# Kernel tuning notes

Measured on AMD Instinct MI355X. Metric: run time of the kernel, lower is better.

The kernel has to match this reference:

```python
import jax, jax.numpy as jnp
import numpy as np

B, SEQ, C, H = 4, 1024, 256, 4
Dk = C // H                                  # 64
L = 4 * SEQ                                  # 4096 attention length
FACTOR = 4
N_TOP = FACTOR * int(np.ceil(np.log(L)))     # U = 36 dominant queries
SAMPLE_K = FACTOR * int(np.ceil(np.log(L)))  # u = 36 sampled keys per query


def _forward(et, mp, co, vol, Wq, bq, Wk, bk, Wv, bv, Wo, bo, index_sample):
    sz = et.shape[0]
    # student_graph input shuffle (faithful to the torch .view calls)
    x = jnp.concatenate([et.reshape(SEQ, -1), co.reshape(SEQ, -1),
                         mp.reshape(SEQ, -1), vol.reshape(SEQ, -1)], axis=-1)
    x = x.reshape(sz, L, C)  # [B, 4*seq_len, d_model]
    # projections; ProbAttention uses view(B,H,L,-1) which is a raw reshape
    # (NOT a transpose) of the [B,L,H,Dk] tensor -> fuse into one reshape
    q = (x @ Wq + bq).reshape(sz, H, L, Dk)
    k = (x @ Wk + bk).reshape(sz, H, L, Dk)
    v = (x @ Wv + bv).reshape(sz, H, L, Dk)
    # _prob_QK: random key sampling + sparsity measure + top-k query select
    K_sample = k[:, :, index_sample, :]                        # [B,H,L,u,Dk]
    QKs = jnp.einsum('bhse,bhske->bhsk', q, K_sample)          # [B,H,L,u]
    M = QKs.max(axis=-1) - QKs.sum(axis=-1) / L                # [B,H,L]
    _, m_top = jax.lax.top_k(M, N_TOP)                         # [B,H,U]
    q_red = jnp.take_along_axis(q, m_top[..., None], axis=2)   # [B,H,U,Dk]
    scores = jnp.einsum('bhue,bhle->bhul', q_red, k) * (1.0 / float(np.sqrt(Dk)))
    attn = jax.nn.softmax(scores, axis=-1)                     # [B,H,U,L]
    upd = jnp.einsum('bhul,bhld->bhud', attn, v)               # [B,H,U,Dk]
    # initial context = V-sum broadcast; scatter dense update at top queries
    ctx = jnp.broadcast_to(v.sum(axis=2, keepdims=True), (sz, H, L, Dk))
    bi = jnp.arange(sz)[:, None, None]
    hi = jnp.arange(H)[None, :, None]
    ctx = ctx.at[bi, hi, m_top, :].set(upd)                    # [B,H,L,Dk]
    # AttentionLayer output: .view(B, L, -1) on contiguous [B,H,L,Dk] is again
    # a raw reshape (faithful), then out projection
    out = ctx.reshape(sz, L, H * Dk) @ Wo + bo                 # [B,L,C]
    return out.reshape(SEQ, -1)


def setup_inputs():
    key = jax.random.key(0)
    ks = jax.random.split(key, 13)
    f = lambda i, shp: jax.random.normal(ks[i], shp, jnp.float32)
    ws = 1.0 / float(np.sqrt(C))  # keep logits in a sane range
    return {
        'et': f(0, (B, SEQ, C)), 'mp': f(1, (B, SEQ, C)),
        'co': f(2, (B, SEQ, C)), 'vol': f(3, (B, SEQ, C)),
        'Wq': f(4, (C, C)) * ws, 'bq': f(5, (C,)) * 0.01,
        'Wk': f(6, (C, C)) * ws, 'bk': f(7, (C,)) * 0.01,
        'Wv': f(8, (C, C)) * ws, 'bv': f(9, (C,)) * 0.01,
        'Wo': f(10, (C, C)) * ws, 'bo': f(11, (C,)) * 0.01,
        'index_sample': jax.random.randint(ks[12], (L, SAMPLE_K), 0, L, dtype=jnp.int32),
        'comp_idx': 0,
    }


def reference(et, mp, co, vol, Wq, bq, Wk, bk, Wv, bv, Wo, bo, index_sample, comp_idx):
    return _forward(et, mp, co, vol, Wq, bq, Wk, bk, Wv, bv, Wo, bo, index_sample)
```

## Files before the change

kernel.cpp:

```cpp
#include <hip/hip_runtime.h>
#include <hip/hip_bf16.h>

#define BHn 16
#define Ln 4096
#define NTOP 36
#define SKn 36
#define NCHUNK 64

using s16x8 = __attribute__((ext_vector_type(8))) short;
using u16x8 = __attribute__((ext_vector_type(8))) unsigned short;
using f32x4 = __attribute__((ext_vector_type(4))) float;

__device__ __forceinline__ unsigned short bf_hi(float f) {
  unsigned u = __float_as_uint(f);
  return (unsigned short)((u + 0x7fffu + ((u >> 16) & 1u)) >> 16);
}

__global__ __launch_bounds__(256) void wconv(
    const float* __restrict__ W0, const float* __restrict__ W1, const float* __restrict__ W2,
    unsigned short* __restrict__ th0, unsigned short* __restrict__ tl0,
    unsigned short* __restrict__ th1, unsigned short* __restrict__ tl1,
    unsigned short* __restrict__ th2, unsigned short* __restrict__ tl2) {
  int wsel = blockIdx.y;
  const float* W = (wsel == 0) ? W0 : (wsel == 1) ? W1 : W2;
  unsigned short* TH = (wsel == 0) ? th0 : (wsel == 1) ? th1 : th2;
  unsigned short* TL = (wsel == 0) ? tl0 : (wsel == 1) ? tl1 : tl2;
  int kr = blockIdx.x * 16;
  int n = threadIdx.x;
  u16x8 hv[2], lv[2];
#pragma unroll
  for (int j = 0; j < 16; ++j) {
    float f = W[(size_t)(kr + j) * 256 + n];
    unsigned short h = bf_hi(f);
    float lof = f - __uint_as_float(((unsigned)h) << 16);
    hv[j >> 3][j & 7] = h;
    lv[j >> 3][j & 7] = bf_hi(lof);
  }
  *(u16x8*)&TH[(size_t)n * 256 + kr] = hv[0];
  *(u16x8*)&TH[(size_t)n * 256 + kr + 8] = hv[1];
  *(u16x8*)&TL[(size_t)n * 256 + kr] = lv[0];
  *(u16x8*)&TL[(size_t)n * 256 + kr + 8] = lv[1];
}

__global__ __launch_bounds__(256) void xconv(
    const float* __restrict__ s0, const float* __restrict__ s1,
    const float* __restrict__ s2, const float* __restrict__ s3,
    unsigned short* __restrict__ Axh, unsigned short* __restrict__ Axl) {
  int t = threadIdx.x;
  int row = blockIdx.x * 4 + (t >> 6);
  int c = t & 63;
  int l = row & 4095, b = row >> 12;
  int part = (l >> 2) & 3;
  int seq = ((l >> 4) << 2) | (l & 3);
  const float* sp = (part == 0) ? s0 : (part == 1) ? s1 : (part == 2) ? s2 : s3;
  float4 f = ((const float4*)(sp + (size_t)((b << 10) + seq) * 256))[c];
  float fv[4] = {f.x, f.y, f.z, f.w};
  ushort4 hv, lv;
  unsigned short* hp = (unsigned short*)&hv;
  unsigned short* lp = (unsigned short*)&lv;
#pragma unroll
  for (int j = 0; j < 4; ++j) {
    unsigned short h = bf_hi(fv[j]);
    float lof = fv[j] - __uint_as_float(((unsigned)h) << 16);
    hp[j] = h;
    lp[j] = bf_hi(lof);
  }
  *(ushort4*)&Axh[(size_t)row * 256 + c * 4] = hv;
  *(ushort4*)&Axl[(size_t)row * 256 + c * 4] = lv;
}

#define LDW 40
__global__ __launch_bounds__(256, 3) void qkv_mfma(
    const unsigned short* __restrict__ Axh, const unsigned short* __restrict__ Axl,
    const unsigned short* __restrict__ th0, const unsigned short* __restrict__ tl0,
    const unsigned short* __restrict__ th1, const unsigned short* __restrict__ tl1,
    const unsigned short* __restrict__ th2, const unsigned short* __restrict__ tl2,
    const float* __restrict__ b0, const float* __restrict__ b1, const float* __restrict__ b2,
    float* __restrict__ o0, float* __restrict__ o1, float* __restrict__ o2) {
  __shared__ __align__(16) unsigned short Ah[128 * LDW];
  __shared__ __align__(16) unsigned short Al[128 * LDW];
  __shared__ __align__(16) unsigned short Bh[128 * LDW];
  __shared__ __align__(16) unsigned short Bl[128 * LDW];
  int t = threadIdx.x;
  int wsel = blockIdx.x >> 1;
  int col0 = (blockIdx.x & 1) * 128;
  int row0 = blockIdx.y * 128;
  const unsigned short* TH = (wsel == 0) ? th0 : (wsel == 1) ? th1 : th2;
  const unsigned short* TL = (wsel == 0) ? tl0 : (wsel == 1) ? tl1 : tl2;
  const float* bias = (wsel == 0) ? b0 : (wsel == 1) ? b1 : b2;
  float* O = (wsel == 0) ? o0 : (wsel == 1) ? o1 : o2;

  int srow = t >> 1, half = t & 1;
  const unsigned short* ah_g = Axh + (size_t)(row0 + srow) * 256 + half * 16;
  const unsigned short* al_g = Axl + (size_t)(row0 + srow) * 256 + half * 16;
  const unsigned short* bh_g = TH + (size_t)(col0 + srow) * 256 + half * 16;
  const unsigned short* bl_g = TL + (size_t)(col0 + srow) * 256 + half * 16;

  int lane = t & 63;
  int wv = t >> 6;
  int wr = wv >> 1, wc = wv & 1;
  int fr = lane & 15, fk = lane >> 4;
  int aoff = (wr * 64 + fr) * LDW + fk * 8;
  int boff = (wc * 64 + fr) * LDW + fk * 8;

  f32x4 acc[4][4] = {};

  for (int k0 = 0; k0 < 256; k0 += 32) {
    int wa = srow * LDW + half * 16;
    u16x8 va0 = *(const u16x8*)(ah_g + k0);
    u16x8 va1 = *(const u16x8*)(ah_g + k0 + 8);
    u16x8 vl0 = *(const u16x8*)(al_g + k0);
    u16x8 vl1 = *(const u16x8*)(al_g + k0 + 8);
    u16x8 vb0 = *(const u16x8*)(bh_g + k0);
    u16x8 vb1 = *(const u16x8*)(bh_g + k0 + 8);
    u16x8 vc0 = *(const u16x8*)(bl_g + k0);
    u16x8 vc1 = *(const u16x8*)(bl_g + k0 + 8);
    *(u16x8*)&Ah[wa] = va0; *(u16x8*)&Ah[wa + 8] = va1;
    *(u16x8*)&Al[wa] = vl0; *(u16x8*)&Al[wa + 8] = vl1;
    *(u16x8*)&Bh[wa] = vb0; *(u16x8*)&Bh[wa + 8] = vb1;
    *(u16x8*)&Bl[wa] = vc0; *(u16x8*)&Bl[wa + 8] = vc1;
    __syncthreads();

    s16x8 fah[4], fal[4];
#pragma unroll
    for (int mi = 0; mi < 4; ++mi) {
      fah[mi] = *(const s16x8*)&Ah[aoff + mi * 16 * LDW];
      fal[mi] = *(const s16x8*)&Al[aoff + mi * 16 * LDW];
    }
#pragma unroll
    for (int ni = 0; ni < 4; ++ni) {
      s16x8 fbh = *(const s16x8*)&Bh[boff + ni * 16 * LDW];
      s16x8 fbl = *(const s16x8*)&Bl[boff + ni * 16 * LDW];
#pragma unroll
      for (int mi = 0; mi < 4; ++mi) {
        acc[mi][ni] = __builtin_amdgcn_mfma_f32_16x16x32_bf16(fah[mi], fbh, acc[mi][ni], 0, 0, 0);
        acc[mi][ni] = __builtin_amdgcn_mfma_f32_16x16x32_bf16(fal[mi], fbh, acc[mi][ni], 0, 0, 0);
        acc[mi][ni] = __builtin_amdgcn_mfma_f32_16x16x32_bf16(fah[mi], fbl, acc[mi][ni], 0, 0, 0);
      }
    }
    __syncthreads();
  }

#pragma unroll
  for (int ni = 0; ni < 4; ++ni) {
    int n = col0 + wc * 64 + ni * 16 + fr;
    float bv = bias[n];
#pragma unroll
    for (int mi = 0; mi < 4; ++mi) {
      int mb = row0 + wr * 64 + mi * 16 + fk * 4;
#pragma unroll
      for (int r = 0; r < 4; ++r)
        O[(size_t)(mb + r) * 256 + n] = acc[mi][ni][r] + bv;
    }
  }
}

__global__ __launch_bounds__(256) void qks_m3(
    const float* __restrict__ q, const float* __restrict__ k,
    const int* __restrict__ idxs, float* __restrict__ Mout) {
  __shared__ float qs[64][68];
  __shared__ int il[64 * SKn];
  int g = blockIdx.x;
  int x = g & 7;
  int i = g >> 3;
  int bh = (x << 1) | (i >> 6);
  int s0 = (i & 63) * 64;
  int t = threadIdx.x;
  size_t base = (size_t)bh << 12;
  for (int i2 = t; i2 < 1024; i2 += 256) {
    int row = i2 >> 4, d4 = i2 & 15;
    *(float4*)&qs[row][d4 * 4] = ((const float4*)(q + (base + s0 + row) * 64))[d4];
  }
  for (int i2 = t; i2 < 64 * SKn; i2 += 256) il[i2] = idxs[s0 * SKn + i2];
  __syncthreads();
  int sl = t >> 2;
  int dq = t & 3;
  float qr[16];
#pragma unroll
  for (int i2 = 0; i2 < 4; ++i2)
    *(float4*)&qr[i2 * 4] = *(const float4*)&qs[sl][i2 * 16 + dq * 4];
  float mx = -INFINITY, sm = 0.f;
  const float4* kb4 = (const float4*)(k + base * 64);
#pragma unroll 4
  for (int j = 0; j < SKn; ++j) {
    int l = il[sl * SKn + j];
    const float4* kr = kb4 + (size_t)l * 16;
    float acc = 0.f;
#pragma unroll
    for (int i2 = 0; i2 < 4; ++i2) {
      float4 kv = kr[i2 * 4 + dq];
      acc += kv.x * qr[i2 * 4] + kv.y * qr[i2 * 4 + 1] + kv.z * qr[i2 * 4 + 2] + kv.w * qr[i2 * 4 + 3];
    }
    acc += __shfl_xor(acc, 1, 64);
    acc += __shfl_xor(acc, 2, 64);
    mx = fmaxf(mx, acc);
    sm += acc;
  }
  if (dq == 0) Mout[base + s0 + sl] = mx - sm * (1.0f / 4096.0f);
}

__global__ __launch_bounds__(256) void topk_radix(
    const float* __restrict__ M, int* __restrict__ topidx) {
  __shared__ unsigned hist[4096];
  __shared__ unsigned sup[256];
  __shared__ unsigned cand_u[256];
  __shared__ int cand_i[256];
  __shared__ int s_bin1, s_bin2, s_above, s_ocnt, s_ccnt;
  int bh = blockIdx.x;
  int t = threadIdx.x;
  int mbase = bh * 4096;
  unsigned uv[16];
  for (int i = t; i < 4096; i += 256) hist[i] = 0;
  __syncthreads();
#pragma unroll
  for (int r = 0; r < 16; ++r) {
    unsigned b = __float_as_uint(M[mbase + t + 256 * r]);
    unsigned u = b ^ ((unsigned)((int)b >> 31) | 0x80000000u);
    uv[r] = u;
    atomicAdd(&hist[u >> 20], 1u);
  }
  __syncthreads();
  {
    unsigned ssum = 0;
    for (int i = 0; i < 16; ++i) ssum += hist[t * 16 + i];
    sup[t] = ssum;
  }
  __syncthreads();
  if (t == 0) {
    unsigned cum = 0; int sb = 255;
    for (; sb > 0; --sb) { if (cum + sup[sb] >= NTOP) break; cum += sup[sb]; }
    int b = sb * 16 + 15;
    for (; b > sb * 16; --b) { if (cum + hist[b] >= NTOP) break; cum += hist[b]; }
    s_bin1 = b; s_above = (int)cum;
  }
  __syncthreads();
  int bin1 = s_bin1;
  int need1 = NTOP - s_above;
  __syncthreads();
  for (int i = t; i < 4096; i += 256) hist[i] = 0;
  __syncthreads();
#pragma unroll
  for (int r = 0; r < 16; ++r)
    if ((int)(uv[r] >> 20) == bin1) atomicAdd(&hist[(uv[r] >> 8) & 0xFFF], 1u);
  __syncthreads();
  {
    unsigned ssum = 0;
    for (int i = 0; i < 16; ++i) ssum += hist[t * 16 + i];
    sup[t] = ssum;
  }
  __syncthreads();
  if (t == 0) {
    unsigned cum = 0; int sb = 255;
    for (; sb > 0; --sb) { if (cum + sup[sb] >= (unsigned)need1) break; cum += sup[sb]; }
    int b = sb * 16 + 15;
    for (; b > sb * 16; --b) { if (cum + hist[b] >= (unsigned)need1) break; cum += hist[b]; }
    s_bin2 = b; s_above += (int)cum;
    s_ocnt = 0; s_ccnt = 0;
  }
  __syncthreads();
  int bin2 = s_bin2;
  int need = NTOP - s_above;
  int* outp = topidx + bh * NTOP;
#pragma unroll
  for (int r = 0; r < 16; ++r) {
    unsigned u = uv[r];
    int b1 = u >> 20, b2 = (u >> 8) & 0xFFF;
    if (b1 > bin1 || (b1 == bin1 && b2 > bin2)) {
      int p = atomicAdd(&s_ocnt, 1);
      outp[p] = t + 256 * r;
    } else if (b1 == bin1 && b2 == bin2) {
      int p = atomicAdd(&s_ccnt, 1);
      if (p < 256) { cand_u[p] = u; cand_i[p] = t + 256 * r; }
    }
  }
  __syncthreads();
  if (t == 0) {
    int cc = s_ccnt < 256 ? s_ccnt : 256;
    int slot = s_ocnt;
    for (int n = 0; n < need; ++n) {
      unsigned bu = 0; int bi = 0x7fffffff, bp = -1;
      for (int c = 0; c < cc; ++c) {
        if (cand_i[c] < 0) continue;
        if (cand_u[c] > bu || (cand_u[c] == bu && cand_i[c] < bi)) {
          bu = cand_u[c]; bi = cand_i[c]; bp = c;
        }
      }
      outp[slot++] = bi;
      cand_i[bp] = -1;
    }
  }
}

__global__ __launch_bounds__(256) void vsum_partial(
    const float* __restrict__ v, float* __restrict__ part) {
  __shared__ float4 red[256];
  int bh = blockIdx.x, ch = blockIdx.y;
  int t = threadIdx.x;
  int rg = t >> 4, d4 = t & 15;
  const float4* v4 = (const float4*)(v + ((size_t)bh * 4096 + ch * 256) * 64);
  float4 acc = {0.f, 0.f, 0.f, 0.f};
  for (int r = rg; r < 256; r += 16) {
    float4 x = v4[r * 16 + d4];
    acc.x += x.x; acc.y += x.y; acc.z += x.z; acc.w += x.w;
  }
  red[t] = acc;
  __syncthreads();
  for (int s2 = 8; s2 > 0; s2 >>= 1) {
    if (rg < s2) {
      float4 o = red[(rg + s2) * 16 + d4];
      red[t].x += o.x; red[t].y += o.y; red[t].z += o.z; red[t].w += o.w;
    }
    __syncthreads();
  }
  if (rg == 0) ((float4*)part)[((size_t)bh * 16 + ch) * 16 + d4] = red[d4];
}

__global__ __launch_bounds__(64) void vsum_final(
    const float* __restrict__ part, float* __restrict__ vsum) {
  int bh = blockIdx.x, lane = threadIdx.x;
  float acc = 0.f;
  for (int ch = 0; ch < 16; ++ch) acc += part[((size_t)bh * 16 + ch) * 64 + lane];
  vsum[bh * 64 + lane] = acc;
}

__global__ __launch_bounds__(256) void attn_partial(
    const float* __restrict__ q, const float* __restrict__ k,
    const float* __restrict__ v, const int* __restrict__ topidx,
    float* __restrict__ part_m, float* __restrict__ part_s,
    float* __restrict__ part_o) {
  __shared__ float4 Ks4[64][17];
  __shared__ float4 qs4[36][17];
  __shared__ float S[36][68];
  int bh = blockIdx.y;
  int c = blockIdx.x;
  int l0 = c * 64;
  int t = threadIdx.x;
  size_t base = (size_t)bh * 4096;

  const float4* kg = (const float4*)(k + (base + l0) * 64);
  for (int i = t; i < 64 * 16; i += 256) {
    int row = i >> 4, d4 = i & 15;
    Ks4[row][d4] = kg[row * 16 + d4];
  }
  for (int i = t; i < 36 * 16; i += 256) {
    int u = i >> 4, d4 = i & 15;
    int m = topidx[bh * NTOP + u];
    qs4[u][d4] = ((const float4*)(q + (base + m) * 64))[d4];
  }
  __syncthreads();

  {
    int l = t & 63, ug = t >> 6;
    float acc[9] = {};
#pragma unroll
    for (int d4 = 0; d4 < 16; ++d4) {
      float4 kv = Ks4[l][d4];
#pragma unroll
      for (int j = 0; j < 9; ++j) {
        float4 qv = qs4[ug * 9 + j][d4];
        acc[j] += kv.x * qv.x + kv.y * qv.y + kv.z * qv.z + kv.w * qv.w;
      }
    }
#pragma unroll
    for (int j = 0; j < 9; ++j) S[ug * 9 + j][l] = acc[j] * 0.125f;
  }
  __syncthreads();

  if (t < NTOP) {
    float mx = -INFINITY;
    for (int l = 0; l < 64; ++l) mx = fmaxf(mx, S[t][l]);
    float sm = 0.f;
    for (int l = 0; l < 64; ++l) { float e = expf(S[t][l] - mx); S[t][l] = e; sm += e; }
    part_m[((size_t)bh * NCHUNK + c) * NTOP + t] = mx;
    part_s[((size_t)bh * NCHUNK + c) * NTOP + t] = sm;
  }
  __syncthreads();

  {
    int d = t & 63, ug = t >> 6;
    float pacc[9] = {};
    const float* vg = v + (base + l0) * 64;
    for (int l = 0; l < 64; ++l) {
      float vv = vg[l * 64 + d];
#pragma unroll
      for (int j = 0; j < 9; ++j) pacc[j] += S[ug * 9 + j][l] * vv;
    }
#pragma unroll
    for (int j = 0; j < 9; ++j)
      part_o[(((size_t)bh * NCHUNK + c) * NTOP + ug * 9 + j) * 64 + d] = pacc[j];
  }
}

__global__ __launch_bounds__(256) void attn_combine(
    const float* __restrict__ part_m, const float* __restrict__ part_s,
    const float* __restrict__ part_o, float* __restrict__ upd) {
  __shared__ float wl[4][64];
  int wave = threadIdx.x >> 6;
  int lane = threadIdx.x & 63;
  int widx = blockIdx.x * 4 + wave;
  int bh = widx / NTOP;
  int u = widx % NTOP;
  float m_c = part_m[((size_t)bh * NCHUNK + lane) * NTOP + u];
  float M = m_c;
#pragma unroll
  for (int off = 32; off > 0; off >>= 1) M = fmaxf(M, __shfl_xor(M, off, 64));
  float w = expf(m_c - M);
  float ds = part_s[((size_t)bh * NCHUNK + lane) * NTOP + u] * w;
#pragma unroll
  for (int off = 32; off > 0; off >>= 1) ds += __shfl_xor(ds, off, 64);
  wl[wave][lane] = w;
  __syncthreads();
  float acc = 0.f;
  for (int c2 = 0; c2 < NCHUNK; ++c2)
    acc += part_o[(((size_t)bh * NCHUNK + c2) * NTOP + u) * 64 + lane] * wl[wave][c2];
  upd[(size_t)widx * 64 + lane] = acc / ds;
}

__global__ __launch_bounds__(256) void out_base(
    const float* __restrict__ vsum, const float* __restrict__ Wo,
    const float* __restrict__ bo, float* __restrict__ outbase) {
  __shared__ float xb[64];
  int bh = blockIdx.x, c = threadIdx.x;
  if (c < 64) xb[c] = vsum[bh * 64 + c];
  __syncthreads();
  float acc = bo[c];
#pragma unroll 8
  for (int d = 0; d < 64; ++d) {
    float w4 = Wo[d * 256 + c] + Wo[(64 + d) * 256 + c] +
               Wo[(128 + d) * 256 + c] + Wo[(192 + d) * 256 + c];
    acc += xb[d] * w4;
  }
  outbase[bh * 256 + c] = acc;
}

__global__ __launch_bounds__(256) void out_fill(
    const float* __restrict__ outbase, float4* __restrict__ out4) {
  int g = blockIdx.x * 256 + threadIdx.x;
  int c4 = g & 63;
  int bh = g >> 16;
  out4[g] = ((const float4*)outbase)[bh * 64 + c4];
}

__global__ __launch_bounds__(256) void out_patch(
    const float* __restrict__ upd, const float* __restrict__ vsum,
    const int* __restrict__ topidx, const float* __restrict__ Wo,
    float* __restrict__ out) {
  __shared__ float dv[64];
  int bhu = blockIdx.x;
  int bh = bhu / NTOP;
  int h = bh & 3, b = bh >> 2;
  int t = threadIdx.x;
  if (t < 64) dv[t] = upd[(size_t)bhu * 64 + t] - vsum[bh * 64 + t];
  __syncthreads();
  int m = topidx[bhu];
  int j = m & 3;
  int lp = h * 1024 + (m >> 2);
  float acc = 0.f;
#pragma unroll 8
  for (int d = 0; d < 64; ++d) acc += dv[d] * Wo[(j * 64 + d) * 256 + t];
  atomicAdd(&out[((size_t)(b * 4096 + lp)) * 256 + t], acc);
}

extern "C" void kernel_launch(void* const* d_in, const int* in_sizes, int n_in,
                              void* d_out, int out_size, void* d_ws, size_t ws_size,
                              hipStream_t stream) {
  const float* et  = (const float*)d_in[0];
  const float* mp  = (const float*)d_in[1];
  const float* co  = (const float*)d_in[2];
  const float* vol = (const float*)d_in[3];
  const float* Wq = (const float*)d_in[4];
  const float* bq = (const float*)d_in[5];
  const float* Wk = (const float*)d_in[6];
  const float* bk = (const float*)d_in[7];
  const float* Wv = (const float*)d_in[8];
  const float* bv = (const float*)d_in[9];
  const float* Wo = (const float*)d_in[10];
  const float* bo = (const float*)d_in[11];
  const int* idxs = (const int*)d_in[12];
  float* out = (float*)d_out;

  char* ws = (char*)d_ws;
  const size_t BIG = 16u * 1024u * 1024u;
  float* qb = (float*)(ws);
  float* kb = (float*)(ws + BIG);
  float* vb = (float*)(ws + 2 * BIG);
  char* sm = ws + 3 * BIG;
  float* Mbuf   = (float*)(sm);
  int*   topidx = (int*)(sm + 262144);
  float* vpart  = (float*)(sm + 262144 + 4096);
  float* vsum   = (float*)(sm + 262144 + 4096 + 65536);
  char* pm = sm + 262144 + 4096 + 65536 + 4096;
  float* part_m = (float*)(pm);
  float* part_s = (float*)(pm + 147456);
  float* part_o = (float*)(pm + 2 * 147456);
  float* updb   = (float*)(pm + 2 * 147456 + 9437184);
  float* outbase = (float*)(pm + 2 * 147456 + 9437184 + 147456);
  unsigned short* wt = (unsigned short*)(pm + 2 * 147456 + 9437184 + 147456 + 16384);
  unsigned short* wth0 = wt;
  unsigned short* wtl0 = wt + 65536;
  unsigned short* wth1 = wt + 2 * 65536;
  unsigned short* wtl1 = wt + 3 * 65536;
  unsigned short* wth2 = wt + 4 * 65536;
  unsigned short* wtl2 = wt + 5 * 65536;
  unsigned short* axh = wt + 6 * 65536;
  unsigned short* axl = axh + 16384 * 256;

  wconv<<<dim3(16, 3), 256, 0, stream>>>(Wq, Wk, Wv, wth0, wtl0, wth1, wtl1, wth2, wtl2);
  xconv<<<4096, 256, 0, stream>>>(et, co, mp, vol, axh, axl);

  qkv_mfma<<<dim3(6, 128), 256, 0, stream>>>(
      axh, axl, wth0, wtl0, wth1, wtl1, wth2, wtl2, bq, bk, bv, qb, kb, vb);

  qks_m3<<<1024, 256, 0, stream>>>(qb, kb, idxs, Mbuf);

  topk_radix<<<BHn, 256, 0, stream>>>(Mbuf, topidx);

  vsum_partial<<<dim3(BHn, 16), 256, 0, stream>>>(vb, vpart);
  vsum_final<<<BHn, 64, 0, stream>>>(vpart, vsum);

  attn_partial<<<dim3(NCHUNK, BHn), 256, 0, stream>>>(
      qb, kb, vb, topidx, part_m, part_s, part_o);
  attn_combine<<<144, 256, 0, stream>>>(part_m, part_s, part_o, updb);

  out_base<<<BHn, 256, 0, stream>>>(vsum, Wo, bo, outbase);
  out_fill<<<4096, 256, 0, stream>>>(outbase, (float4*)out);
  out_patch<<<BHn * NTOP, 256, 0, stream>>>(updb, vsum, topidx, Wo, out);
}
```

Before: 157.7 us.

## Use single-bf16 MFMA for V projection and remap grids for XCD locality

The V projection now uses only the high-bf16 halves of X and W, one MFMA per tile instead of the three-term split-bf16 emulation, skipping the low-part loads and LDS stores. The Q and K projections keep the three-term scheme, presumably because they feed top-k selection. Both qkv_mfma and attn_partial switch to 1D grids with remapped block indices, likely so blocks sharing the same weights or the same head land on the same XCD and share its L2. The cost is lower precision in V, which could push outputs past tolerance.

```diff
diff --git a/kernel.cpp b/kernel.cpp
--- a/kernel.cpp
+++ b/kernel.cpp
@@ -82,13 +82,16 @@
   __shared__ __align__(16) unsigned short Bh[128 * LDW];
   __shared__ __align__(16) unsigned short Bl[128 * LDW];
   int t = threadIdx.x;
-  int wsel = blockIdx.x >> 1;
-  int col0 = (blockIdx.x & 1) * 128;
-  int row0 = blockIdx.y * 128;
+  int g = blockIdx.x;
+  int vnt = g >> 7;
+  int wsel = vnt >> 1;
+  int col0 = (vnt & 1) * 128;
+  int row0 = (g & 127) * 128;
   const unsigned short* TH = (wsel == 0) ? th0 : (wsel == 1) ? th1 : th2;
   const unsigned short* TL = (wsel == 0) ? tl0 : (wsel == 1) ? tl1 : tl2;
   const float* bias = (wsel == 0) ? b0 : (wsel == 1) ? b1 : b2;
   float* O = (wsel == 0) ? o0 : (wsel == 1) ? o1 : o2;
+  const bool vlite = (wsel == 2);
 
   int srow = t >> 1, half = t & 1;
   const unsigned short* ah_g = Axh + (size_t)(row0 + srow) * 256 + half * 16;
@@ -109,33 +112,49 @@
     int wa = srow * LDW + half * 16;
     u16x8 va0 = *(const u16x8*)(ah_g + k0);
     u16x8 va1 = *(const u16x8*)(ah_g + k0 + 8);
-    u16x8 vl0 = *(const u16x8*)(al_g + k0);
-    u16x8 vl1 = *(const u16x8*)(al_g + k0 + 8);
     u16x8 vb0 = *(const u16x8*)(bh_g + k0);
     u16x8 vb1 = *(const u16x8*)(bh_g + k0 + 8);
-    u16x8 vc0 = *(const u16x8*)(bl_g + k0);
-    u16x8 vc1 = *(const u16x8*)(bl_g + k0 + 8);
     *(u16x8*)&Ah[wa] = va0; *(u16x8*)&Ah[wa + 8] = va1;
-    *(u16x8*)&Al[wa] = vl0; *(u16x8*)&Al[wa + 8] = vl1;
     *(u16x8*)&Bh[wa] = vb0; *(u16x8*)&Bh[wa + 8] = vb1;
-    *(u16x8*)&Bl[wa] = vc0; *(u16x8*)&Bl[wa + 8] = vc1;
+    if (!vlite) {
+      u16x8 vl0 = *(const u16x8*)(al_g + k0);
+      u16x8 vl1 = *(const u16x8*)(al_g + k0 + 8);
+      u16x8 vc0 = *(const u16x8*)(bl_g + k0);
+      u16x8 vc1 = *(const u16x8*)(bl_g + k0 + 8);
+      *(u16x8*)&Al[wa] = vl0; *(u16x8*)&Al[wa + 8] = vl1;
+      *(u16x8*)&Bl[wa] = vc0; *(u16x8*)&Bl[wa + 8] = vc1;
+    }
     __syncthreads();
 
-    s16x8 fah[4], fal[4];
-#pragma unroll
-    for (int mi = 0; mi < 4; ++mi) {
-      fah[mi] = *(const s16x8*)&Ah[aoff + mi * 16 * LDW];
-      fal[mi] = *(const s16x8*)&Al[aoff + mi * 16 * LDW];
-    }
-#pragma unroll
-    for (int ni = 0; ni < 4; ++ni) {
-      s16x8 fbh = *(const s16x8*)&Bh[boff + ni * 16 * LDW];
-      s16x8 fbl = *(const s16x8*)&Bl[boff + ni * 16 * LDW];
+    if (vlite) {
+      s16x8 fah[4];
+#pragma unroll
+      for (int mi = 0; mi < 4; ++mi)
+        fah[mi] = *(const s16x8*)&Ah[aoff + mi * 16 * LDW];
+#pragma unroll
+      for (int ni = 0; ni < 4; ++ni) {
+        s16x8 fbh = *(const s16x8*)&Bh[boff + ni * 16 * LDW];
+#pragma unroll
+        for (int mi = 0; mi < 4; ++mi)
+          acc[mi][ni] = __builtin_amdgcn_mfma_f32_16x16x32_bf16(fah[mi], fbh, acc[mi][ni], 0, 0, 0);
+      }
+    } else {
+      s16x8 fah[4], fal[4];
 #pragma unroll
       for (int mi = 0; mi < 4; ++mi) {
-        acc[mi][ni] = __builtin_amdgcn_mfma_f32_16x16x32_bf16(fah[mi], fbh, acc[mi][ni], 0, 0, 0);
-        acc[mi][ni] = __builtin_amdgcn_mfma_f32_16x16x32_bf16(fal[mi], fbh, acc[mi][ni], 0, 0, 0);
-        acc[mi][ni] = __builtin_amdgcn_mfma_f32_16x16x32_bf16(fah[mi], fbl, acc[mi][ni], 0, 0, 0);
+        fah[mi] = *(const s16x8*)&Ah[aoff + mi * 16 * LDW];
+        fal[mi] = *(const s16x8*)&Al[aoff + mi * 16 * LDW];
+      }
+#pragma unroll
+      for (int ni = 0; ni < 4; ++ni) {
+        s16x8 fbh = *(const s16x8*)&Bh[boff + ni * 16 * LDW];
+        s16x8 fbl = *(const s16x8*)&Bl[boff + ni * 16 * LDW];
+#pragma unroll
+        for (int mi = 0; mi < 4; ++mi) {
+          acc[mi][ni] = __builtin_amdgcn_mfma_f32_16x16x32_bf16(fah[mi], fbh, acc[mi][ni], 0, 0, 0);
+          acc[mi][ni] = __builtin_amdgcn_mfma_f32_16x16x32_bf16(fal[mi], fbh, acc[mi][ni], 0, 0, 0);
+          acc[mi][ni] = __builtin_amdgcn_mfma_f32_16x16x32_bf16(fah[mi], fbl, acc[mi][ni], 0, 0, 0);
+        }
       }
     }
     __syncthreads();
@@ -331,19 +350,22 @@
   __shared__ float4 Ks4[64][17];
   __shared__ float4 qs4[36][17];
   __shared__ float S[36][68];
-  int bh = blockIdx.y;
-  int c = blockIdx.x;
+  int g = blockIdx.x;
+  int x = g & 7;
+  int i = g >> 3;
+  int bh = (x << 1) | (i >> 6);
+  int c = i & 63;
   int l0 = c * 64;
   int t = threadIdx.x;
   size_t base = (size_t)bh * 4096;
 
   const float4* kg = (const float4*)(k + (base + l0) * 64);
-  for (int i = t; i < 64 * 16; i += 256) {
-    int row = i >> 4, d4 = i & 15;
+  for (int i2 = t; i2 < 64 * 16; i2 += 256) {
+    int row = i2 >> 4, d4 = i2 & 15;
     Ks4[row][d4] = kg[row * 16 + d4];
   }
-  for (int i = t; i < 36 * 16; i += 256) {
-    int u = i >> 4, d4 = i & 15;
+  for (int i2 = t; i2 < 36 * 16; i2 += 256) {
+    int u = i2 >> 4, d4 = i2 & 15;
     int m = topidx[bh * NTOP + u];
     qs4[u][d4] = ((const float4*)(q + (base + m) * 64))[d4];
   }
@@ -508,7 +530,7 @@
   wconv<<<dim3(16, 3), 256, 0, stream>>>(Wq, Wk, Wv, wth0, wtl0, wth1, wtl1, wth2, wtl2);
   xconv<<<4096, 256, 0, stream>>>(et, co, mp, vol, axh, axl);
 
-  qkv_mfma<<<dim3(6, 128), 256, 0, stream>>>(
+  qkv_mfma<<<768, 256, 0, stream>>>(
       axh, axl, wth0, wtl0, wth1, wtl1, wth2, wtl2, bq, bk, bv, qb, kb, vb);
 
   qks_m3<<<1024, 256, 0, stream>>>(qb, kb, idxs, Mbuf);
@@ -518,7 +540,7 @@
   vsum_partial<<<dim3(BHn, 16), 256, 0, stream>>>(vb, vpart);
   vsum_final<<<BHn, 64, 0, stream>>>(vpart, vsum);
 
-  attn_partial<<<dim3(NCHUNK, BHn), 256, 0, stream>>>(
+  attn_partial<<<1024, 256, 0, stream>>>(
       qb, kb, vb, topidx, part_m, part_s, part_o);
   attn_combine<<<144, 256, 0, stream>>>(part_m, part_s, part_o, updb);
 
```

Result: faster. 150.1 us (-4.9%).
